# Kernel optimization log

Hardware: AMD Instinct MI355X
Metric: run time of the kernel (lower is better)

The kernel has to match this reference:

```python
import jax, jax.numpy as jnp
import numpy as np

B, N, DIM, HEADS, DIM_HEAD = 2, 2048, 1024, 16, 64
INNER = HEADS * DIM_HEAD
LN_EPS = 1e-5


def setup_inputs() -> dict:
    key = jax.random.key(0)
    k1, k2, k3 = jax.random.split(key, 3)
    x = jax.random.normal(k1, (B, N, DIM), dtype=jnp.float32)
    ln_w = jnp.ones((DIM,), dtype=jnp.float32)
    ln_b = jnp.zeros((DIM,), dtype=jnp.float32)
    w_qkv = jax.random.normal(k2, (DIM, 3 * INNER), dtype=jnp.float32) * (DIM ** -0.5)
    w_out = jax.random.normal(k3, (INNER, DIM), dtype=jnp.float32) * (INNER ** -0.5)
    return {"x": x, "ln_w": ln_w, "ln_b": ln_b, "w_qkv": w_qkv, "w_out": w_out}


def reference(x, ln_w, ln_b, w_qkv, w_out):
    scale = DIM_HEAD ** -0.5
    # LayerNorm over last dim
    mu = jnp.mean(x, axis=-1, keepdims=True)
    var = jnp.var(x, axis=-1, keepdims=True)
    xn = (x - mu) / jnp.sqrt(var + LN_EPS) * ln_w + ln_b
    # qkv projection, split, reshape to b h n d
    qkv = xn @ w_qkv  # [B, N, 3*INNER]
    q, k, v = jnp.split(qkv, 3, axis=-1)
    def to_heads(t):
        return t.reshape(B, N, HEADS, DIM_HEAD).transpose(0, 2, 1, 3)
    q, k, v = to_heads(q) * scale, to_heads(k), to_heads(v)
    # scores + causal mask (triu with offset 1 masked)
    sim = jnp.einsum('bhid,bhjd->bhij', q, k)  # [B, H, N, N]
    causal_mask = jnp.triu(jnp.ones((N, N), dtype=bool), k=1)
    sim = jnp.where(causal_mask, -jnp.finfo(sim.dtype).max, sim)
    attn = jax.nn.softmax(sim, axis=-1)
    out = jnp.einsum('bhij,bhjd->bhid', attn, v)  # [B, H, N, D]
    out = out.transpose(0, 2, 1, 3).reshape(B, N, INNER)
    return out @ w_out
```

## Files before the change

kernel.cpp:

```cpp
#include <hip/hip_runtime.h>
#include <stdint.h>

#define BATCH 2
#define NSEQ  2048
#define DIMC  1024
#define NHEAD 16
#define DHEAD 64
#define QKVN  3072
#define MROWS 4096

typedef __attribute__((ext_vector_type(8))) unsigned short u16x8;
typedef __attribute__((ext_vector_type(4))) unsigned short u16x4;
typedef __attribute__((ext_vector_type(8))) short          bf16x8;
typedef __attribute__((ext_vector_type(4))) short          s16x4;
typedef __attribute__((ext_vector_type(4))) float          f32x4;

#define F32_PROBE 0x3F800000u
#define QSCALE 0.18033688f

__device__ __forceinline__ float b2f(unsigned short u) {
  union { unsigned int i; float f; } c; c.i = ((unsigned int)u) << 16; return c.f;
}
__device__ __forceinline__ unsigned short f2b(float f) {
  unsigned int u = __float_as_uint(f);
  return (unsigned short)((u + 0x7fffu + ((u >> 16) & 1u)) >> 16);
}
__device__ __forceinline__ float fast_exp2(float x) {
  return __builtin_amdgcn_exp2f(x);
}
__device__ __forceinline__ void async16(const unsigned short* g, unsigned short* s) {
  __builtin_amdgcn_global_load_lds(
      (const __attribute__((address_space(1))) unsigned int*)g,
      (__attribute__((address_space(3))) unsigned int*)s, 16, 0, 0);
}
__device__ __forceinline__ f32x4 mfma_k16(s16x4 a, s16x4 b, f32x4 c) {
#if __has_builtin(__builtin_amdgcn_mfma_f32_16x16x16bf16_1k)
  return __builtin_amdgcn_mfma_f32_16x16x16bf16_1k(a, b, c, 0, 0, 0);
#else
  asm("v_mfma_f32_16x16x16_bf16 %0, %1, %2, %0" : "+v"(c) : "v"(a), "v"(b));
  return c;
#endif
}

__device__ __forceinline__ void tr_tile(const void* __restrict__ in,
                                        unsigned short* __restrict__ out,
                                        int R, int C, int r0, int c0, bool f32,
                                        int t, unsigned short (*tile)[33],
                                        int scale_below) {
  int tx = t & 31, ty = t >> 5;
  float sc = (c0 < scale_below) ? QSCALE : 1.0f;
  if (f32) {
    #pragma unroll
    for (int i = 0; i < 32; i += 8)
      tile[ty + i][tx] = f2b(((const float*)in)[(size_t)(r0 + ty + i) * C + c0 + tx] * sc);
  } else {
    #pragma unroll
    for (int i = 0; i < 32; i += 8)
      tile[ty + i][tx] = f2b(b2f(((const unsigned short*)in)[(size_t)(r0 + ty + i) * C + c0 + tx]) * sc);
  }
  __syncthreads();
  #pragma unroll
  for (int i = 0; i < 32; i += 8)
    out[(size_t)(c0 + ty + i) * R + r0 + tx] = tile[tx][ty + i];
}

__global__ __launch_bounds__(256) void prep_kernel(const void* __restrict__ x,
                                                   const void* __restrict__ w,
                                                   const void* __restrict__ bb,
                                                   unsigned short* __restrict__ xn,
                                                   const void* __restrict__ w_qkv,
                                                   unsigned short* __restrict__ wqkvT,
                                                   const void* __restrict__ w_out,
                                                   unsigned short* __restrict__ woutT,
                                                   const unsigned int* __restrict__ probe) {
  __shared__ unsigned short tile[32][33];
  __shared__ float red[8];
  bool f32 = (*probe == F32_PROBE);
  int bid = blockIdx.x, t = threadIdx.x;

  if (bid < MROWS) {
    int row = bid;
    float v0, v1, v2, v3, w0, w1, w2, w3, bb0, bb1, bb2, bb3;
    if (f32) {
      const float* xr = (const float*)x + (size_t)row * DIMC;
      float4 xv = *(const float4*)(xr + t * 4);
      v0 = xv.x; v1 = xv.y; v2 = xv.z; v3 = xv.w;
      float4 wv = *(const float4*)((const float*)w + t * 4);
      w0 = wv.x; w1 = wv.y; w2 = wv.z; w3 = wv.w;
      float4 bv = *(const float4*)((const float*)bb + t * 4);
      bb0 = bv.x; bb1 = bv.y; bb2 = bv.z; bb3 = bv.w;
    } else {
      const unsigned short* xr = (const unsigned short*)x + (size_t)row * DIMC;
      u16x4 xv = *(const u16x4*)(xr + t * 4);
      v0 = b2f(xv[0]); v1 = b2f(xv[1]); v2 = b2f(xv[2]); v3 = b2f(xv[3]);
      u16x4 wv = *(const u16x4*)((const unsigned short*)w + t * 4);
      w0 = b2f(wv[0]); w1 = b2f(wv[1]); w2 = b2f(wv[2]); w3 = b2f(wv[3]);
      u16x4 bv = *(const u16x4*)((const unsigned short*)bb + t * 4);
      bb0 = b2f(bv[0]); bb1 = b2f(bv[1]); bb2 = b2f(bv[2]); bb3 = b2f(bv[3]);
    }
    float s = v0 + v1 + v2 + v3;
    float q = v0 * v0 + v1 * v1 + v2 * v2 + v3 * v3;
    #pragma unroll
    for (int off = 1; off < 64; off <<= 1) { s += __shfl_xor(s, off); q += __shfl_xor(q, off); }
    int wv_ = t >> 6;
    if ((t & 63) == 0) { red[wv_] = s; red[4 + wv_] = q; }
    __syncthreads();
    s = red[0] + red[1] + red[2] + red[3];
    q = red[4] + red[5] + red[6] + red[7];
    float mu  = s * (1.0f / DIMC);
    float var = q * (1.0f / DIMC) - mu * mu;
    float rstd = rsqrtf(var + 1e-5f);
    u16x4 o;
    o[0] = f2b((v0 - mu) * rstd * w0 + bb0);
    o[1] = f2b((v1 - mu) * rstd * w1 + bb1);
    o[2] = f2b((v2 - mu) * rstd * w2 + bb2);
    o[3] = f2b((v3 - mu) * rstd * w3 + bb3);
    *(u16x4*)(xn + (size_t)row * DIMC + t * 4) = o;
  } else if (bid < MROWS + 3072) {
    int tid = bid - MROWS;
    tr_tile(w_qkv, wqkvT, DIMC, QKVN, (tid / 96) * 32, (tid % 96) * 32, f32, t, tile, 1024);
  } else {
    int tid = bid - (MROWS + 3072);
    tr_tile(w_out, woutT, DIMC, DIMC, (tid >> 5) * 32, (tid & 31) * 32, f32, t, tile, 0);
  }
}

__global__ __launch_bounds__(256) void transpose_kernel(const void* __restrict__ in,
                                                        unsigned short* __restrict__ out,
                                                        int R, int C,
                                                        const unsigned int* __restrict__ probe) {
  __shared__ unsigned short tile[32][33];
  bool f32 = (*probe == F32_PROBE);
  int t = threadIdx.x;
  tr_tile(in, out, R, C, blockIdx.y * 32, blockIdx.x * 32, f32, t, tile, 0);
}

__device__ __forceinline__ void ldA8(bf16x8 (&dst)[8], const unsigned short* base,
                                     int off, int ch0, int ch1) {
  #pragma unroll
  for (int mi = 0; mi < 4; ++mi) {
    dst[mi * 2 + 0] = *(const bf16x8*)&base[off + mi * 1024 + ch0];
    dst[mi * 2 + 1] = *(const bf16x8*)&base[off + mi * 1024 + ch1];
  }
}
__device__ __forceinline__ void ldB3(bf16x8 (&dst)[3], const unsigned short* base,
                                     int off, int ch) {
  #pragma unroll
  for (int ni = 0; ni < 3; ++ni)
    dst[ni] = *(const bf16x8*)&base[off + ni * 1024 + ch];
}
__device__ __forceinline__ void mfma12(f32x4 (&acc)[4][6], const bf16x8 (&a)[8],
                                       const bf16x8 (&b)[3], int C, int kh) {
  #pragma unroll
  for (int mi = 0; mi < 4; ++mi)
    #pragma unroll
    for (int ni = 0; ni < 3; ++ni)
      acc[mi][C * 3 + ni] = __builtin_amdgcn_mfma_f32_16x16x32_bf16(
          a[mi * 2 + kh], b[ni], acc[mi][C * 3 + ni], 0, 0, 0);
}

#define SB    asm volatile("s_barrier" ::: "memory")
#define WVM4  asm volatile("s_waitcnt vmcnt(4)" ::: "memory")
#define WVM0  asm volatile("s_waitcnt vmcnt(0)" ::: "memory")
#define WLG0  asm volatile("s_waitcnt lgkmcnt(0)" ::: "memory")
#define PRIO1 __builtin_amdgcn_s_setprio(1)
#define PRIO0 __builtin_amdgcn_s_setprio(0)
#define STG(gp, g, k0, sb) async16((gp) + (size_t)(g) * 65536 + (k0), (sb) + (g) * 4096 + t8)

__global__ __launch_bounds__(512) void gemm1_8p(const unsigned short* __restrict__ A,
                                                const unsigned short* __restrict__ Bt,
                                                unsigned short* __restrict__ C,
                                                unsigned short* __restrict__ vt_out) {
  __shared__ unsigned short lds[57344];
  unsigned short* A0b = lds;
  unsigned short* A1b = lds + 16384;
  unsigned short* B0b = lds + 32768;
  unsigned short* B1b = lds + 45056;

  int t = threadIdx.x;
  int lane = t & 63, wv = t >> 6;
  int l16 = lane & 15, quad = lane >> 4;
  int wr = wv >> 1, wc = wv & 1;

  int bid = blockIdx.x;
  int xcd = bid & 7, rr = bid >> 3;
  int bx = (xcd & 3) * 4 + (rr >> 3);
  int by = (xcd >> 2) * 8 + (rr & 7);
  int bm = bx * 256, bn = by * 192;

  int rl = t >> 3;
  int sc8 = (((t & 7) ^ (rl & 7)) << 3);
  int t8 = t * 8;
  const unsigned short* Ag = A  + (size_t)(bm + rl) * 1024 + sc8;
  const unsigned short* Bg = Bt + (size_t)(bn + rl) * 1024 + sc8;

  int aoff = (wr * 64 + l16) * 64;
  int boff = (wc * 96 + l16) * 64;
  int ch0 = ((quad ^ (l16 & 7)) << 3);
  int ch1 = (((quad + 4) ^ (l16 & 7)) << 3);

  f32x4 acc[4][6] = {};
  bf16x8 ar[8], bcE[3], bcO[3];

  STG(Ag, 0, 0, A0b); STG(Ag, 1, 0, A0b); STG(Ag, 2, 0, A0b); STG(Ag, 3, 0, A0b);
  STG(Bg, 0, 0, B0b); STG(Bg, 1, 0, B0b); STG(Bg, 2, 0, B0b);
  STG(Ag, 0, 64, A1b); STG(Ag, 1, 64, A1b); STG(Ag, 2, 64, A1b); STG(Ag, 3, 64, A1b);
  WVM4;
  SB;

  for (int i = 0; i < 8; ++i) {
    const int k_b1 = (2 * i + 1) * 64;
    const int k_n0 = ((2 * i + 2) & 15) * 64;
    const int k_n1 = ((2 * i + 3) & 15) * 64;

    ldA8(ar, A0b, aoff, ch0, ch1);
    ldB3(bcE, B0b, boff, ch0);
    STG(Bg, 0, k_b1, B1b); STG(Bg, 1, k_b1, B1b);
    SB; WLG0; PRIO1; mfma12(acc, ar, bcE, 0, 0); PRIO0; SB;
    ldB3(bcO, B0b, boff + 3072, ch0);
    STG(Bg, 2, k_b1, B1b);
    SB; WLG0; PRIO1; mfma12(acc, ar, bcO, 1, 0); PRIO0; SB;
    ldB3(bcE, B0b, boff, ch1);
    STG(Ag, 0, k_n0, A0b); STG(Ag, 1, k_n0, A0b);
    SB; WLG0; PRIO1; mfma12(acc, ar, bcE, 0, 1); PRIO0; SB;
    ldB3(bcO, B0b, boff + 3072, ch1);
    STG(Ag, 2, k_n0, A0b); STG(Ag, 3, k_n0, A0b);
    WVM4;
    SB; WLG0; PRIO1; mfma12(acc, ar, bcO, 1, 1); PRIO0; SB;

    ldA8(ar, A1b, aoff, ch0, ch1);
    ldB3(bcE, B1b, boff, ch0);
    STG(Bg, 0, k_n0, B0b); STG(Bg, 1, k_n0, B0b);
    SB; WLG0; PRIO1; mfma12(acc, ar, bcE, 0, 0); PRIO0; SB;
    ldB3(bcO, B1b, boff + 3072, ch0);
    STG(Bg, 2, k_n0, B0b);
    SB; WLG0; PRIO1; mfma12(acc, ar, bcO, 1, 0); PRIO0; SB;
    ldB3(bcE, B1b, boff, ch1);
    STG(Ag, 0, k_n1, A1b); STG(Ag, 1, k_n1, A1b);
    SB; WLG0; PRIO1; mfma12(acc, ar, bcE, 0, 1); PRIO0; SB;
    ldB3(bcO, B1b, boff + 3072, ch1);
    STG(Ag, 2, k_n1, A1b); STG(Ag, 3, k_n1, A1b);
    WVM4;
    SB; WLG0; PRIO1; mfma12(acc, ar, bcO, 1, 1); PRIO0; SB;
  }

  #pragma unroll
  for (int rf = 0; rf < 4; ++rf)
    #pragma unroll
    for (int cf = 0; cf < 6; ++cf) {
      int gr0 = bm + wr * 64 + rf * 16 + quad * 4;
      int gc  = bn + wc * 96 + cf * 16 + l16;
      if (gc >= 2048) {
        int hh = (gc >> 6) & 15;
        int dd = gc & 63;
        int bb2 = gr0 >> 11;
        int n0  = gr0 & 2047;
        u16x4 pk;
        #pragma unroll
        for (int r = 0; r < 4; r++) pk[r] = f2b(acc[rf][cf][r]);
        *(u16x4*)&vt_out[(((size_t)(bb2 * 16 + hh) * 64 + dd) << 11) + n0] = pk;
      } else {
        #pragma unroll
        for (int r = 0; r < 4; r++)
          C[(size_t)(gr0 + r) * QKVN + gc] = f2b(acc[rf][cf][r]);
      }
    }
}

__device__ __forceinline__ void ld4(bf16x8 (&dst)[4], const unsigned short* base,
                                    int off, int ch0, int ch1) {
  #pragma unroll
  for (int m = 0; m < 2; ++m) {
    dst[m * 2 + 0] = *(const bf16x8*)&base[off + m * 1024 + ch0];
    dst[m * 2 + 1] = *(const bf16x8*)&base[off + m * 1024 + ch1];
  }
}
__device__ __forceinline__ void mfma8(f32x4 (&acc)[4][4], const bf16x8 (&a)[4],
                                      const bf16x8 (&b)[4], int R, int C) {
  #pragma unroll
  for (int kh = 0; kh < 2; ++kh)
    #pragma unroll
    for (int m = 0; m < 2; ++m)
      #pragma unroll
      for (int n = 0; n < 2; ++n)
        acc[R * 2 + m][C * 2 + n] = __builtin_amdgcn_mfma_f32_16x16x32_bf16(
            a[m * 2 + kh], b[n * 2 + kh], acc[R * 2 + m][C * 2 + n], 0, 0, 0);
}
#define STG2A(g, k0, sb) async16(Ag + (size_t)(g) * 32 * QKVN + (k0), (sb) + (g) * 2048 + t8)
#define STG2B(g, k0, sb) async16(Bg + (size_t)(g) * 32 * 1024 + (k0), (sb) + (g) * 2048 + t8)

__global__ __launch_bounds__(256) void gemm2_8p(const unsigned short* __restrict__ A,
                                                const unsigned short* __restrict__ Bt,
                                                void* __restrict__ Cv,
                                                const unsigned int* __restrict__ probe) {
  __shared__ unsigned short lds[32768];
  unsigned short* A0b = lds;
  unsigned short* A1b = lds + 8192;
  unsigned short* B0b = lds + 16384;
  unsigned short* B1b = lds + 24576;

  int t = threadIdx.x;
  int lane = t & 63, wv = t >> 6;
  int l16 = lane & 15, quad = lane >> 4;
  int wr = wv >> 1, wc = wv & 1;

  int bid = blockIdx.x;
  int xcd = bid & 7, rr = bid >> 3;
  int bx = xcd * 4 + (rr >> 3);
  int by = rr & 7;
  int bm = bx * 128, bn = by * 128;

  int rl = t >> 3;
  int sc8 = (((t & 7) ^ (rl & 7)) << 3);
  int t8 = t * 8;
  const unsigned short* Ag = A  + (size_t)(bm + rl) * QKVN + sc8;
  const unsigned short* Bg = Bt + (size_t)(bn + rl) * 1024 + sc8;

  int aoff = (wr * 64 + l16) * 64;
  int boff = (wc * 64 + l16) * 64;
  int ch0 = ((quad ^ (l16 & 7)) << 3);
  int ch1 = (((quad + 4) ^ (l16 & 7)) << 3);

  f32x4 acc[4][4] = {};
  bf16x8 arE[4], arO[4], bcE[4], bcO[4];

  STG2A(0, 0, A0b); STG2A(1, 0, A0b); STG2A(2, 0, A0b); STG2A(3, 0, A0b);
  STG2B(0, 0, B0b); STG2B(1, 0, B0b); STG2B(2, 0, B0b); STG2B(3, 0, B0b);
  STG2A(0, 64, A1b); STG2A(1, 64, A1b); STG2A(2, 64, A1b); STG2A(3, 64, A1b);
  WVM4;
  SB;

  for (int i = 0; i < 8; ++i) {
    const int k_b1 = (2 * i + 1) * 64;
    const int k_n0 = ((2 * i + 2) & 15) * 64;
    const int k_n1 = ((2 * i + 3) & 15) * 64;

    ld4(arE, A0b, aoff, ch0, ch1);
    ld4(bcE, B0b, boff, ch0, ch1);
    STG2B(0, k_b1, B1b); STG2B(1, k_b1, B1b);
    SB; WLG0; PRIO1; mfma8(acc, arE, bcE, 0, 0); PRIO0; SB;
    ld4(arO, A0b, aoff + 2048, ch0, ch1);
    STG2B(2, k_b1, B1b); STG2B(3, k_b1, B1b);
    SB; WLG0; PRIO1; mfma8(acc, arO, bcE, 1, 0); PRIO0; SB;
    ld4(bcO, B0b, boff + 2048, ch0, ch1);
    STG2A(0, k_n0, A0b); STG2A(1, k_n0, A0b);
    SB; WLG0; PRIO1; mfma8(acc, arE, bcO, 0, 1); PRIO0; SB;
    STG2A(2, k_n0, A0b); STG2A(3, k_n0, A0b);
    WVM4;
    SB; PRIO1; mfma8(acc, arO, bcO, 1, 1); PRIO0; SB;

    ld4(arE, A1b, aoff, ch0, ch1);
    ld4(bcE, B1b, boff, ch0, ch1);
    STG2B(0, k_n0, B0b); STG2B(1, k_n0, B0b);
    SB; WLG0; PRIO1; mfma8(acc, arE, bcE, 0, 0); PRIO0; SB;
    ld4(arO, A1b, aoff + 2048, ch0, ch1);
    STG2B(2, k_n0, B0b); STG2B(3, k_n0, B0b);
    SB; WLG0; PRIO1; mfma8(acc, arO, bcE, 1, 0); PRIO0; SB;
    ld4(bcO, B1b, boff + 2048, ch0, ch1);
    STG2A(0, k_n1, A1b); STG2A(1, k_n1, A1b);
    SB; WLG0; PRIO1; mfma8(acc, arE, bcO, 0, 1); PRIO0; SB;
    STG2A(2, k_n1, A1b); STG2A(3, k_n1, A1b);
    WVM4;
    SB; PRIO1; mfma8(acc, arO, bcO, 1, 1); PRIO0; SB;
  }

  bool f32out = (*probe == F32_PROBE);
  #pragma unroll
  for (int rf = 0; rf < 4; ++rf)
    #pragma unroll
    for (int cf = 0; cf < 4; ++cf) {
      int gr0 = bm + wr * 64 + rf * 16 + quad * 4;
      int gc  = bn + wc * 64 + cf * 16 + l16;
      #pragma unroll
      for (int r = 0; r < 4; r++) {
        if (f32out) ((float*)Cv)[(size_t)(gr0 + r) * DIMC + gc] = acc[rf][cf][r];
        else ((unsigned short*)Cv)[(size_t)(gr0 + r) * DIMC + gc] = f2b(acc[rf][cf][r]);
      }
    }
}

#define OSW(d, c) ((d) * 64 + ((((c)) ^ ((d) & 15)) << 2))

__global__ __launch_bounds__(256, 3) void attn_v8(unsigned short* __restrict__ qkv,
                                                  const unsigned short* __restrict__ vt) {
  __shared__ unsigned short lds[16384];

  int t = threadIdx.x;
  int lane = t & 63, w = t >> 6;
  int l16 = lane & 15, quad = lane >> 4;
  int id = blockIdx.x;
  int xcd = id & 7, jj = id >> 3;
  int bh = xcd + ((jj & 3) << 3);
  int qt = 31 - (jj >> 2);
  int b = bh >> 4, h = bh & 15;
  unsigned short* qbase = qkv + (size_t)(b * NSEQ) * QKVN + h * DHEAD;
  const unsigned short* kbase = qbase + 1024;
  const unsigned short* vtb = vt + (size_t)bh * DHEAD * NSEQ;
  int q0 = qt * 64;

  unsigned short* wbase = lds + w * 4096;
  int lane8 = lane * 8;
  int kr = lane >> 3;
  int kchunk = (lane & 7) ^ kr;
  size_t kgo = (size_t)(w * 16 + kr) * QKVN + kchunk * 8;
  int vd = lane >> 1;
  int vh = (lane & 1) ^ ((vd >> 2) & 1);
  size_t vgo = (size_t)vd * NSEQ + w * 16 + vh * 8;

#define STAGE_V8(j0, Kb, Vb) do { \
    async16(kbase + (size_t)(j0) * QKVN + kgo,       (Kb) + lane8);       \
    async16(kbase + (size_t)((j0) + 8) * QKVN + kgo, (Kb) + 512 + lane8); \
    async16(vtb + (size_t)(j0) + vgo,                (Vb) + lane8);       \
    async16(vtb + (size_t)(j0) + 32 * NSEQ + vgo,    (Vb) + 512 + lane8); } while (0)

  bf16x8 bq0[4], bq1[4];
  #pragma unroll
  for (int qb = 0; qb < 4; qb++) {
    const unsigned short* qp = qbase + (size_t)(q0 + qb * 16 + l16) * QKVN + quad * 8;
    bq0[qb] = *(const bf16x8*)(qp);
    bq1[qb] = *(const bf16x8*)(qp + 32);
  }

  float l4[4] = {0.f, 0.f, 0.f, 0.f};
  f32x4 o[4][4] = {};

  STAGE_V8(0, wbase, wbase + 2048);

  for (int jt = 0; jt <= qt; jt++) {
    unsigned short* Kb = wbase + (jt & 1) * 1024;
    unsigned short* Vb = wbase + 2048 + (jt & 1) * 1024;

    if (jt < qt) {
      int j0n = (jt + 1) * 64;
      unsigned short* Kn = wbase + ((jt + 1) & 1) * 1024;
      unsigned short* Vn = wbase + 2048 + ((jt + 1) & 1) * 1024;
      STAGE_V8(j0n, Kn, Vn);
      WVM4;
    } else {
      WVM0;
    }

    bf16x8 ak0 = *(const bf16x8*)&Kb[l16 * 64 + ((quad ^ (l16 & 7)) << 3)];
    bf16x8 ak1 = *(const bf16x8*)&Kb[l16 * 64 + (((quad + 4) ^ (l16 & 7)) << 3)];
    f32x4 sv[4];
    PRIO1;
    #pragma unroll
    for (int qb = 0; qb < 4; qb++) {
      f32x4 s = {-32.0f, -32.0f, -32.0f, -32.0f};
      s = __builtin_amdgcn_mfma_f32_16x16x32_bf16(ak0, bq0[qb], s, 0, 0, 0);
      s = __builtin_amdgcn_mfma_f32_16x16x32_bf16(ak1, bq1[qb], s, 0, 0, 0);
      sv[qb] = s;
    }
    PRIO0;

    s16x4 pa[4];
    #pragma unroll
    for (int qb = 0; qb < 4; qb++) {
      float p0 = fast_exp2(sv[qb][0]);
      float p1 = fast_exp2(sv[qb][1]);
      float p2 = fast_exp2(sv[qb][2]);
      float p3 = fast_exp2(sv[qb][3]);
      if (jt == qt) {
        int jl = w * 16 + quad * 4, ql = qb * 16 + l16;
        if (jl + 0 > ql) p0 = 0.f;
        if (jl + 1 > ql) p1 = 0.f;
        if (jl + 2 > ql) p2 = 0.f;
        if (jl + 3 > ql) p3 = 0.f;
      }
      l4[qb] += (p0 + p1) + (p2 + p3);
      union { unsigned int u[2]; s16x4 v; } cc;
      asm("v_cvt_pk_bf16_f32 %0, %1, %2" : "=v"(cc.u[0]) : "v"(p0), "v"(p1));
      asm("v_cvt_pk_bf16_f32 %0, %1, %2" : "=v"(cc.u[1]) : "v"(p2), "v"(p3));
      pa[qb] = cc.v;
    }

    PRIO1;
    #pragma unroll
    for (int db = 0; db < 4; db++) {
      int d = db * 16 + l16;
      int hh = (quad >> 1) ^ ((l16 >> 2) & 1);
      u16x4 vb = *(const u16x4*)&Vb[d * 16 + hh * 8 + (quad & 1) * 4];
      union { u16x4 u; s16x4 s; } vc; vc.u = vb;
      #pragma unroll
      for (int qb = 0; qb < 4; qb++)
        o[qb][db] = mfma_k16(pa[qb], vc.s, o[qb][db]);
    }
    PRIO0;
  }

  #pragma unroll
  for (int qb = 0; qb < 4; qb++) {
    l4[qb] += __shfl_xor(l4[qb], 16);
    l4[qb] += __shfl_xor(l4[qb], 32);
  }
  __syncthreads();
  float* f = (float*)lds;
  if (quad == 0) {
    #pragma unroll
    for (int qb = 0; qb < 4; qb++) f[w * 64 + qb * 16 + l16] = l4[qb];
  }
  __syncthreads();
  #pragma unroll
  for (int qb = 0; qb < 4; qb++)
    l4[qb] = (f[qb * 16 + l16] + f[64 + qb * 16 + l16]) +
             (f[128 + qb * 16 + l16] + f[192 + qb * 16 + l16]);
  __syncthreads();

  float* r0 = f;
  float* r1 = f + 4096;
  if (w == 1 || w == 3) {
    float* rg = (w == 1) ? r0 : r1;
    #pragma unroll
    for (int qb = 0; qb < 4; qb++)
      #pragma unroll
      for (int db = 0; db < 4; db++)
        *(f32x4*)&rg[OSW(db * 16 + l16, qb * 4 + quad)] = o[qb][db];
  }
  __syncthreads();
  if (w == 0 || w == 2) {
    float* rg = (w == 0) ? r0 : r1;
    #pragma unroll
    for (int qb = 0; qb < 4; qb++)
      #pragma unroll
      for (int db = 0; db < 4; db++)
        o[qb][db] += *(const f32x4*)&rg[OSW(db * 16 + l16, qb * 4 + quad)];
  }
  __syncthreads();
  if (w == 2) {
    #pragma unroll
    for (int qb = 0; qb < 4; qb++)
      #pragma unroll
      for (int db = 0; db < 4; db++)
        *(f32x4*)&r0[OSW(db * 16 + l16, qb * 4 + quad)] = o[qb][db];
  }
  __syncthreads();
  if (w == 0) {
    #pragma unroll
    for (int qb = 0; qb < 4; qb++) {
      #pragma unroll
      for (int db = 0; db < 4; db++)
        o[qb][db] += *(const f32x4*)&r0[OSW(db * 16 + l16, qb * 4 + quad)];
      #pragma unroll
      for (int r = 0; r < 4; r++) {
        float lr = __shfl(l4[qb], (lane & 48) | (quad * 4 + r));
        float inv = 1.0f / lr;
        int row = q0 + qb * 16 + quad * 4 + r;
        #pragma unroll
        for (int db = 0; db < 4; db++)
          qbase[(size_t)row * QKVN + db * 16 + l16] = f2b(o[qb][db][r] * inv);
      }
    }
  }
}

extern "C" void kernel_launch(void* const* d_in, const int* in_sizes, int n_in,
                              void* d_out, int out_size, void* d_ws, size_t ws_size,
                              hipStream_t stream) {
  const void* x     = d_in[0];
  const void* ln_w  = d_in[1];
  const void* ln_b  = d_in[2];
  const void* w_qkv = d_in[3];
  const void* w_out = d_in[4];
  const unsigned int* probe = (const unsigned int*)d_in[1];

  unsigned short* wqkvT = (unsigned short*)d_ws;
  unsigned short* qkv   = wqkvT + (size_t)QKVN * DIMC;
  unsigned short* xn    = (unsigned short*)d_out;
  size_t base_e  = (size_t)QKVN * DIMC + (size_t)MROWS * QKVN;
  size_t vt_e    = (size_t)BATCH * NHEAD * DHEAD * NSEQ;
  size_t wout_e  = (size_t)DIMC * DIMC;
  bool fit_vt  = ws_size >= (base_e + vt_e) * 2;
  bool fit_all = ws_size >= (base_e + vt_e + wout_e) * 2;
  unsigned short* vtp   = fit_vt ? qkv + (size_t)MROWS * QKVN
                                 : ((unsigned short*)d_out) + ((size_t)4 * 1024 * 1024);
  unsigned short* woutT = fit_all ? vtp + vt_e : wqkvT;

  int prep_blocks = MROWS + 3072 + (fit_all ? 1024 : 0);
  prep_kernel<<<prep_blocks, 256, 0, stream>>>(x, ln_w, ln_b, xn, w_qkv, wqkvT,
                                               w_out, fit_all ? woutT : nullptr, probe);
  gemm1_8p<<<dim3(256), 512, 0, stream>>>(xn, wqkvT, qkv, vtp);
  if (!fit_all)
    transpose_kernel<<<dim3(DIMC / 32, DIMC / 32), 256, 0, stream>>>(w_out, woutT, DIMC, DIMC, probe);
  attn_v8<<<dim3(1024), 256, 0, stream>>>(qkv, vtp);
  gemm2_8p<<<dim3(256), 256, 0, stream>>>(qkv, woutT, d_out, probe);
}
```

Baseline: 163.3 us.

## Software-pipeline attention softmax/PV one tile behind QK and split A-fragment loads

The attention kernel now computes QK scores for tile jt while doing exp/convert and the PV MFMAs for tile jt-1. K and V staging are split so V is fetched a tile later, and the causal mask moves to an epilogue that handles the last tile. Occupancy hint drops from 3 to 2 blocks per CU to make room for the extra live score registers. In gemm1 the A-fragment LDS reads are split into two halves, so the second half is read just before the MFMAs that need it, lowering register pressure and spreading LDS traffic.

```diff
diff --git a/kernel.cpp b/kernel.cpp
--- a/kernel.cpp
+++ b/kernel.cpp
@@ -135,13 +135,11 @@
   tr_tile(in, out, R, C, blockIdx.y * 32, blockIdx.x * 32, f32, t, tile, 0);
 }
 
-__device__ __forceinline__ void ldA8(bf16x8 (&dst)[8], const unsigned short* base,
-                                     int off, int ch0, int ch1) {
-  #pragma unroll
-  for (int mi = 0; mi < 4; ++mi) {
-    dst[mi * 2 + 0] = *(const bf16x8*)&base[off + mi * 1024 + ch0];
-    dst[mi * 2 + 1] = *(const bf16x8*)&base[off + mi * 1024 + ch1];
-  }
+__device__ __forceinline__ void ldA4(bf16x8 (&dst)[8], int kh, const unsigned short* base,
+                                     int off, int ch) {
+  #pragma unroll
+  for (int mi = 0; mi < 4; ++mi)
+    dst[mi * 2 + kh] = *(const bf16x8*)&base[off + mi * 1024 + ch];
 }
 __device__ __forceinline__ void ldB3(bf16x8 (&dst)[3], const unsigned short* base,
                                      int off, int ch) {
@@ -161,6 +159,7 @@
 
 #define SB    asm volatile("s_barrier" ::: "memory")
 #define WVM4  asm volatile("s_waitcnt vmcnt(4)" ::: "memory")
+#define WVM2  asm volatile("s_waitcnt vmcnt(2)" ::: "memory")
 #define WVM0  asm volatile("s_waitcnt vmcnt(0)" ::: "memory")
 #define WLG0  asm volatile("s_waitcnt lgkmcnt(0)" ::: "memory")
 #define PRIO1 __builtin_amdgcn_s_setprio(1)
@@ -213,10 +212,11 @@
     const int k_n0 = ((2 * i + 2) & 15) * 64;
     const int k_n1 = ((2 * i + 3) & 15) * 64;
 
-    ldA8(ar, A0b, aoff, ch0, ch1);
+    ldA4(ar, 0, A0b, aoff, ch0);
     ldB3(bcE, B0b, boff, ch0);
     STG(Bg, 0, k_b1, B1b); STG(Bg, 1, k_b1, B1b);
     SB; WLG0; PRIO1; mfma12(acc, ar, bcE, 0, 0); PRIO0; SB;
+    ldA4(ar, 1, A0b, aoff, ch1);
     ldB3(bcO, B0b, boff + 3072, ch0);
     STG(Bg, 2, k_b1, B1b);
     SB; WLG0; PRIO1; mfma12(acc, ar, bcO, 1, 0); PRIO0; SB;
@@ -228,10 +228,11 @@
     WVM4;
     SB; WLG0; PRIO1; mfma12(acc, ar, bcO, 1, 1); PRIO0; SB;
 
-    ldA8(ar, A1b, aoff, ch0, ch1);
+    ldA4(ar, 0, A1b, aoff, ch0);
     ldB3(bcE, B1b, boff, ch0);
     STG(Bg, 0, k_n0, B0b); STG(Bg, 1, k_n0, B0b);
     SB; WLG0; PRIO1; mfma12(acc, ar, bcE, 0, 0); PRIO0; SB;
+    ldA4(ar, 1, A1b, aoff, ch1);
     ldB3(bcO, B1b, boff + 3072, ch0);
     STG(Bg, 2, k_n0, B0b);
     SB; WLG0; PRIO1; mfma12(acc, ar, bcO, 1, 0); PRIO0; SB;
@@ -379,9 +380,12 @@
     }
 }
 
+__device__ __forceinline__ int swz(int row, int chunk) {
+  return row * 64 + ((chunk ^ (row & 7)) << 3);
+}
 #define OSW(d, c) ((d) * 64 + ((((c)) ^ ((d) & 15)) << 2))
 
-__global__ __launch_bounds__(256, 3) void attn_v8(unsigned short* __restrict__ qkv,
+__global__ __launch_bounds__(256, 2) void attn_v9(unsigned short* __restrict__ qkv,
                                                   const unsigned short* __restrict__ vt) {
   __shared__ unsigned short lds[16384];
 
@@ -407,9 +411,10 @@
   int vh = (lane & 1) ^ ((vd >> 2) & 1);
   size_t vgo = (size_t)vd * NSEQ + w * 16 + vh * 8;
 
-#define STAGE_V8(j0, Kb, Vb) do { \
+#define STAGE_K9(j0, Kb) do { \
     async16(kbase + (size_t)(j0) * QKVN + kgo,       (Kb) + lane8);       \
-    async16(kbase + (size_t)((j0) + 8) * QKVN + kgo, (Kb) + 512 + lane8); \
+    async16(kbase + (size_t)((j0) + 8) * QKVN + kgo, (Kb) + 512 + lane8); } while (0)
+#define STAGE_V9(j0, Vb) do { \
     async16(vtb + (size_t)(j0) + vgo,                (Vb) + lane8);       \
     async16(vtb + (size_t)(j0) + 32 * NSEQ + vgo,    (Vb) + 512 + lane8); } while (0)
 
@@ -423,63 +428,91 @@
 
   float l4[4] = {0.f, 0.f, 0.f, 0.f};
   f32x4 o[4][4] = {};
-
-  STAGE_V8(0, wbase, wbase + 2048);
+  f32x4 svp[4];
+
+  STAGE_K9(0, wbase);
 
   for (int jt = 0; jt <= qt; jt++) {
     unsigned short* Kb = wbase + (jt & 1) * 1024;
-    unsigned short* Vb = wbase + 2048 + (jt & 1) * 1024;
-
-    if (jt < qt) {
-      int j0n = (jt + 1) * 64;
-      unsigned short* Kn = wbase + ((jt + 1) & 1) * 1024;
-      unsigned short* Vn = wbase + 2048 + ((jt + 1) & 1) * 1024;
-      STAGE_V8(j0n, Kn, Vn);
-      WVM4;
-    } else {
-      WVM0;
-    }
+
+    if (jt < qt) STAGE_K9((jt + 1) * 64, wbase + ((jt + 1) & 1) * 1024);
+    STAGE_V9(jt * 64, wbase + 2048 + (jt & 1) * 1024);
+    if (jt == qt) { WVM2; }
+    else         { WVM4; }
 
     bf16x8 ak0 = *(const bf16x8*)&Kb[l16 * 64 + ((quad ^ (l16 & 7)) << 3)];
     bf16x8 ak1 = *(const bf16x8*)&Kb[l16 * 64 + (((quad + 4) ^ (l16 & 7)) << 3)];
-    f32x4 sv[4];
+    f32x4 svc[4];
     PRIO1;
     #pragma unroll
     for (int qb = 0; qb < 4; qb++) {
       f32x4 s = {-32.0f, -32.0f, -32.0f, -32.0f};
       s = __builtin_amdgcn_mfma_f32_16x16x32_bf16(ak0, bq0[qb], s, 0, 0, 0);
       s = __builtin_amdgcn_mfma_f32_16x16x32_bf16(ak1, bq1[qb], s, 0, 0, 0);
-      sv[qb] = s;
+      svc[qb] = s;
     }
     PRIO0;
 
+    if (jt > 0) {
+      s16x4 pa[4];
+      #pragma unroll
+      for (int qb = 0; qb < 4; qb++) {
+        float p0 = fast_exp2(svp[qb][0]);
+        float p1 = fast_exp2(svp[qb][1]);
+        float p2 = fast_exp2(svp[qb][2]);
+        float p3 = fast_exp2(svp[qb][3]);
+        l4[qb] += (p0 + p1) + (p2 + p3);
+        union { unsigned int u[2]; s16x4 v; } cc;
+        asm("v_cvt_pk_bf16_f32 %0, %1, %2" : "=v"(cc.u[0]) : "v"(p0), "v"(p1));
+        asm("v_cvt_pk_bf16_f32 %0, %1, %2" : "=v"(cc.u[1]) : "v"(p2), "v"(p3));
+        pa[qb] = cc.v;
+      }
+      unsigned short* Vp = wbase + 2048 + ((jt - 1) & 1) * 1024;
+      PRIO1;
+      #pragma unroll
+      for (int db = 0; db < 4; db++) {
+        int d = db * 16 + l16;
+        int hh = (quad >> 1) ^ ((l16 >> 2) & 1);
+        u16x4 vb = *(const u16x4*)&Vp[d * 16 + hh * 8 + (quad & 1) * 4];
+        union { u16x4 u; s16x4 s; } vc; vc.u = vb;
+        #pragma unroll
+        for (int qb = 0; qb < 4; qb++)
+          o[qb][db] = mfma_k16(pa[qb], vc.s, o[qb][db]);
+      }
+      PRIO0;
+    }
+
+    #pragma unroll
+    for (int qb = 0; qb < 4; qb++) svp[qb] = svc[qb];
+  }
+
+  WVM0;
+  {
     s16x4 pa[4];
     #pragma unroll
     for (int qb = 0; qb < 4; qb++) {
-      float p0 = fast_exp2(sv[qb][0]);
-      float p1 = fast_exp2(sv[qb][1]);
-      float p2 = fast_exp2(sv[qb][2]);
-      float p3 = fast_exp2(sv[qb][3]);
-      if (jt == qt) {
-        int jl = w * 16 + quad * 4, ql = qb * 16 + l16;
-        if (jl + 0 > ql) p0 = 0.f;
-        if (jl + 1 > ql) p1 = 0.f;
-        if (jl + 2 > ql) p2 = 0.f;
-        if (jl + 3 > ql) p3 = 0.f;
-      }
+      float p0 = fast_exp2(svp[qb][0]);
+      float p1 = fast_exp2(svp[qb][1]);
+      float p2 = fast_exp2(svp[qb][2]);
+      float p3 = fast_exp2(svp[qb][3]);
+      int jl = w * 16 + quad * 4, ql = qb * 16 + l16;
+      if (jl + 0 > ql) p0 = 0.f;
+      if (jl + 1 > ql) p1 = 0.f;
+      if (jl + 2 > ql) p2 = 0.f;
+      if (jl + 3 > ql) p3 = 0.f;
       l4[qb] += (p0 + p1) + (p2 + p3);
       union { unsigned int u[2]; s16x4 v; } cc;
       asm("v_cvt_pk_bf16_f32 %0, %1, %2" : "=v"(cc.u[0]) : "v"(p0), "v"(p1));
       asm("v_cvt_pk_bf16_f32 %0, %1, %2" : "=v"(cc.u[1]) : "v"(p2), "v"(p3));
       pa[qb] = cc.v;
     }
-
+    unsigned short* Vp = wbase + 2048 + (qt & 1) * 1024;
     PRIO1;
     #pragma unroll
     for (int db = 0; db < 4; db++) {
       int d = db * 16 + l16;
       int hh = (quad >> 1) ^ ((l16 >> 2) & 1);
-      u16x4 vb = *(const u16x4*)&Vb[d * 16 + hh * 8 + (quad & 1) * 4];
+      u16x4 vb = *(const u16x4*)&Vp[d * 16 + hh * 8 + (quad & 1) * 4];
       union { u16x4 u; s16x4 s; } vc; vc.u = vb;
       #pragma unroll
       for (int qb = 0; qb < 4; qb++)
@@ -581,6 +614,6 @@
   gemm1_8p<<<dim3(256), 512, 0, stream>>>(xn, wqkvT, qkv, vtp);
   if (!fit_all)
     transpose_kernel<<<dim3(DIMC / 32, DIMC / 32), 256, 0, stream>>>(w_out, woutT, DIMC, DIMC, probe);
-  attn_v8<<<dim3(1024), 256, 0, stream>>>(qkv, vtp);
+  attn_v9<<<dim3(1024), 256, 0, stream>>>(qkv, vtp);
   gemm2_8p<<<dim3(256), 256, 0, stream>>>(qkv, woutT, d_out, probe);
 }
```

New measurement: 166.8 us. 2.1% more time.
